# Kernel optimization log

Measured on AMD Instinct MI355X. Metric: run time of the kernel, lower is better.

## Reference

```python
import math
import jax, jax.numpy as jnp
import numpy as np

EMBED_DIM = 512
NUM_HEADS = 8
QHD = 32          # query/key head dim
PHD = 4           # pos head dim (unused: use_pos_scores forced False in source)
IN_PROJ = (QHD + QHD + PHD) * NUM_HEADS  # 544
S = 2048
B = 4
MASK_VAL = -1000.0  # source uses masked_fill(mask, -1000)


def sinusoidal_pe(T, d):
    # PE(pos,2i)=sin(pos/10000^(2i/d)), PE(pos,2i+1)=cos(...)
    pos = jnp.arange(T, dtype=jnp.float32)[:, None]
    div = jnp.exp(jnp.arange(0, d, 2, dtype=jnp.float32) * (-math.log(10000.0) / d))
    pe = jnp.zeros((T, d), jnp.float32)
    pe = pe.at[:, 0::2].set(jnp.sin(pos * div))
    pe = pe.at[:, 1::2].set(jnp.cos(pos * div))
    return pe


def setup_inputs() -> dict:
    key = jax.random.key(0)
    ks = jax.random.split(key, 4)
    scale = QHD ** (-0.25) / math.sqrt(EMBED_DIM)  # ScaledLinear initial_scale folded in
    return {
        "query": jax.random.normal(ks[0], (S, B, EMBED_DIM), jnp.float32),
        "key": jax.random.normal(ks[1], (S, B, EMBED_DIM), jnp.float32),
        "Wq": jax.random.normal(ks[2], (EMBED_DIM, IN_PROJ), jnp.float32) * scale,
        "bq": jnp.zeros((IN_PROJ,), jnp.float32),
        "Wk": jax.random.normal(ks[3], (EMBED_DIM, IN_PROJ), jnp.float32) * scale,
        "bk": jnp.zeros((IN_PROJ,), jnp.float32),
        "key_padding_mask": jnp.zeros((B, S), bool),
        "attn_mask": jnp.zeros((S, S), bool),
    }


def reference(query, key, Wq, bq, Wk, bk, key_padding_mask, attn_mask):
    q_len, batch, _ = query.shape
    k_len = key.shape[0]
    # key_proj over full in_proj_dim (k slice taken below, p slice is dead code)
    k_proj = key @ Wk + bk                       # (K, B, IN_PROJ)
    # decoder_pos: add sinusoidal PE to query (dropout inactive at eval)
    pe = sinusoidal_pe(q_len, EMBED_DIM)
    q_proj = (query + pe[:, None, :]) @ Wq + bq  # (Q, B, IN_PROJ)
    qd = QHD * NUM_HEADS
    q = q_proj[..., :qd].reshape(q_len, batch, NUM_HEADS, QHD)
    k = k_proj[..., qd:2 * qd].reshape(k_len, batch, NUM_HEADS, QHD)
    # attn_scores: (num_heads, batch, q_len, k_len)
    scores = jnp.einsum("qbhd,kbhd->hbqk", q, k)
    scores = jnp.where(attn_mask[None, None, :, :], MASK_VAL, scores)
    scores = jnp.where(key_padding_mask[None, :, None, :], MASK_VAL, scores)
    return jax.nn.softmax(scores, axis=-1)
```

## Files before the change

kernel.cpp:

```cpp
#include <hip/hip_runtime.h>
#include <math.h>

typedef __bf16 bf16_t;
typedef __bf16 bf16x8 __attribute__((ext_vector_type(8)));
typedef __bf16 bf16x4v __attribute__((ext_vector_type(4)));
typedef float f32x4 __attribute__((ext_vector_type(4)));

#define MFMA16x16(a, b, c) __builtin_amdgcn_mfma_f32_16x16x32_bf16((a), (b), (c), 0, 0, 0)

#define MASK_VAL -1000.0f
#define EXP_SHIFT 20.0f


__global__ __launch_bounds__(256) void prep_qpe(const float* __restrict__ query,
                                                bf16_t* __restrict__ qin) {
    int idx = blockIdx.x * 256 + threadIdx.x;
    int s = idx >> 8;
    int i = idx & 255;
    int e = i * 2;
    const float C = 9.210340371976184f / 512.0f;
    float freq = __expf(-(float)e * C);
    float ang = (float)s * freq;
    float sv, cv;
    sincosf(ang, &sv, &cv);
    #pragma unroll
    for (int b = 0; b < 4; b++) {
        int base = ((s * 4 + b) << 9) + e;
        qin[base]     = (bf16_t)(query[base] + sv);
        qin[base + 1] = (bf16_t)(query[base + 1] + cv);
    }
}

__global__ __launch_bounds__(256) void prep_kcast(const float* __restrict__ key,
                                                  bf16_t* __restrict__ kin) {
    int idx = blockIdx.x * 256 + threadIdx.x;
    float4 v = ((const float4*)key)[idx];
    bf16x4v o;
    o.x = (bf16_t)v.x; o.y = (bf16_t)v.y; o.z = (bf16_t)v.z; o.w = (bf16_t)v.w;
    ((bf16x4v*)kin)[idx] = o;
}

__global__ __launch_bounds__(256) void prep_wt(const float* __restrict__ Wq,
                                               const float* __restrict__ Wk,
                                               bf16_t* __restrict__ wqt,
                                               bf16_t* __restrict__ wkt) {
    int idx = blockIdx.x * 256 + threadIdx.x;
    int t = idx & 131071;
    int j = t >> 9, e = t & 511;
    if (idx < 131072) wqt[t] = (bf16_t)Wq[e * 544 + j];
    else              wkt[t] = (bf16_t)Wk[e * 544 + 256 + j];
}

__global__ __launch_bounds__(256) void mask_any(const uint4* __restrict__ am,
                                                const uint4* __restrict__ kpm,
                                                int* __restrict__ flag) {
    int idx = blockIdx.x * 256 + threadIdx.x;
    unsigned int v = 0;
    if (idx < 262144) { uint4 x = am[idx]; v = x.x | x.y | x.z | x.w; }
    else if (idx < 262656) { uint4 x = kpm[idx - 262144]; v = x.x | x.y | x.z | x.w; }
    if (v) atomicOr(flag, 1);
}

__global__ __launch_bounds__(256) void proj_gemm(const bf16_t* __restrict__ A,
                                                 const bf16_t* __restrict__ Bt,
                                                 const float* __restrict__ bias,
                                                 bf16_t* __restrict__ Out) {
    int lane = threadIdx.x & 63;
    int wave = threadIdx.x >> 6;
    int wm = wave & 1, wn = wave >> 1;
    int m0 = blockIdx.x * 64 + wm * 32;
    int n0 = blockIdx.y * 64 + wn * 32;
    int lrow = lane & 15, quad = lane >> 4;
    f32x4 acc00 = {0.f, 0.f, 0.f, 0.f};
    f32x4 acc01 = acc00, acc10 = acc00, acc11 = acc00;
    const bf16_t* Ab = A + (size_t)(m0 + lrow) * 512 + quad * 8;
    const bf16_t* Bb = Bt + (size_t)(n0 + lrow) * 512 + quad * 8;
    #pragma unroll 4
    for (int k0 = 0; k0 < 512; k0 += 32) {
        bf16x8 a0 = *(const bf16x8*)(Ab + k0);
        bf16x8 a1 = *(const bf16x8*)(Ab + 16 * 512 + k0);
        bf16x8 b0 = *(const bf16x8*)(Bb + k0);
        bf16x8 b1 = *(const bf16x8*)(Bb + 16 * 512 + k0);
        acc00 = MFMA16x16(a0, b0, acc00);
        acc01 = MFMA16x16(a0, b1, acc01);
        acc10 = MFMA16x16(a1, b0, acc10);
        acc11 = MFMA16x16(a1, b1, acc11);
    }
    #pragma unroll
    for (int i = 0; i < 2; i++) {
        #pragma unroll
        for (int j = 0; j < 2; j++) {
            f32x4 acc = (i == 0) ? (j == 0 ? acc00 : acc01) : (j == 0 ? acc10 : acc11);
            int col = n0 + j * 16 + lrow;
            float bv = bias[col];
            int h = col >> 5, d = col & 31;
            #pragma unroll
            for (int r = 0; r < 4; r++) {
                int row = m0 + i * 16 + quad * 4 + r;
                int s = row >> 2, bb = row & 3;
                Out[(size_t)((h * 4 + bb) * 2048 + s) * 32 + d] = (bf16_t)(acc[r] + bv);
            }
        }
    }
}

template <bool MASKED>
__device__ __forceinline__ void attn_core(const bf16_t* __restrict__ Qb,
                                          const bf16_t* __restrict__ Kb,
                                          const unsigned char* __restrict__ am,
                                          const unsigned char* __restrict__ kpm,
                                          float* __restrict__ out) {
    int lane = threadIdx.x & 63;
    int wave = threadIdx.x >> 6;
    int hb = blockIdx.y;
    int b = hb & 3;
    int q0 = blockIdx.x * 64 + wave * 16;
    int lrow = lane & 15, quad = lane >> 4;
    bf16x8 afrag = *(const bf16x8*)(Qb + (size_t)(hb * 2048 + q0 + lrow) * 32 + quad * 8);
    const bf16_t* kbase = Kb + (size_t)hb * 2048 * 32;

    float m[4] = {-1e30f, -1e30f, -1e30f, -1e30f};
    float l[4] = {0.f, 0.f, 0.f, 0.f};
    #pragma unroll 2
    for (int t0 = 0; t0 < 2048; t0 += 16) {
        bf16x8 bfrag = *(const bf16x8*)(kbase + (size_t)(t0 + lrow) * 32 + quad * 8);
        f32x4 acc = {0.f, 0.f, 0.f, 0.f};
        acc = MFMA16x16(afrag, bfrag, acc);
        int col = t0 + lrow;
        bool kp = MASKED ? (kpm[b * 2048 + col] != 0) : false;
        #pragma unroll
        for (int r = 0; r < 4; r++) {
            float s = acc[r];
            if (MASKED) {
                int row = q0 + quad * 4 + r;
                if (kp || am[(size_t)row * 2048 + col]) s = MASK_VAL;
            }
            m[r] = fmaxf(m[r], s);
            l[r] += __expf(s - EXP_SHIFT);
        }
    }
    #pragma unroll
    for (int off = 1; off < 16; off <<= 1) {
        #pragma unroll
        for (int r = 0; r < 4; r++) {
            m[r] = fmaxf(m[r], __shfl_xor(m[r], off));
            l[r] += __shfl_xor(l[r], off);
        }
    }
    float M[4], INV[4];
    bool need = false;
    #pragma unroll
    for (int r = 0; r < 4; r++) need = need || (l[r] == 0.0f) || (m[r] > 80.0f);
    if (__any(need)) {
        float l2[4] = {0.f, 0.f, 0.f, 0.f};
        for (int t0 = 0; t0 < 2048; t0 += 16) {
            bf16x8 bfrag = *(const bf16x8*)(kbase + (size_t)(t0 + lrow) * 32 + quad * 8);
            f32x4 acc = {0.f, 0.f, 0.f, 0.f};
            acc = MFMA16x16(afrag, bfrag, acc);
            int col = t0 + lrow;
            bool kp = MASKED ? (kpm[b * 2048 + col] != 0) : false;
            #pragma unroll
            for (int r = 0; r < 4; r++) {
                float s = acc[r];
                if (MASKED) {
                    int row = q0 + quad * 4 + r;
                    if (kp || am[(size_t)row * 2048 + col]) s = MASK_VAL;
                }
                l2[r] += __expf(s - m[r]);
            }
        }
        #pragma unroll
        for (int off = 1; off < 16; off <<= 1) {
            #pragma unroll
            for (int r = 0; r < 4; r++) l2[r] += __shfl_xor(l2[r], off);
        }
        #pragma unroll
        for (int r = 0; r < 4; r++) { M[r] = m[r]; INV[r] = 1.0f / l2[r]; }
    } else {
        #pragma unroll
        for (int r = 0; r < 4; r++) { M[r] = EXP_SHIFT; INV[r] = 1.0f / l[r]; }
    }
    float* obase = out + (size_t)hb * 2048 * 2048;
    #pragma unroll 2
    for (int t0 = 0; t0 < 2048; t0 += 16) {
        bf16x8 bfrag = *(const bf16x8*)(kbase + (size_t)(t0 + lrow) * 32 + quad * 8);
        f32x4 acc = {0.f, 0.f, 0.f, 0.f};
        acc = MFMA16x16(afrag, bfrag, acc);
        int col = t0 + lrow;
        bool kp = MASKED ? (kpm[b * 2048 + col] != 0) : false;
        #pragma unroll
        for (int r = 0; r < 4; r++) {
            float s = acc[r];
            int row = q0 + quad * 4 + r;
            if (MASKED) {
                if (kp || am[(size_t)row * 2048 + col]) s = MASK_VAL;
            }
            float o = __expf(s - M[r]) * INV[r];
            __builtin_nontemporal_store(o, obase + (size_t)row * 2048 + col);
        }
    }
}

__global__ __launch_bounds__(256) void attn_kernel(const bf16_t* __restrict__ Qb,
                                                   const bf16_t* __restrict__ Kb,
                                                   const unsigned char* __restrict__ am,
                                                   const unsigned char* __restrict__ kpm,
                                                   const int* __restrict__ flag,
                                                   float* __restrict__ out) {
    if (*flag) attn_core<true>(Qb, Kb, am, kpm, out);
    else       attn_core<false>(Qb, Kb, am, kpm, out);
}

extern "C" void kernel_launch(void* const* d_in, const int* in_sizes, int n_in,
                              void* d_out, int out_size, void* d_ws, size_t ws_size,
                              hipStream_t stream) {
    const float* query = (const float*)d_in[0];
    const float* key   = (const float*)d_in[1];
    const float* Wq    = (const float*)d_in[2];
    const float* bq    = (const float*)d_in[3];
    const float* Wk    = (const float*)d_in[4];
    const float* bk    = (const float*)d_in[5];
    const unsigned char* kpm = (const unsigned char*)d_in[6];
    const unsigned char* am  = (const unsigned char*)d_in[7];
    float* out = (float*)d_out;

    char* ws = (char*)d_ws;
    bf16_t* qin = (bf16_t*)(ws);
    bf16_t* kin = (bf16_t*)(ws + (8u << 20));
    bf16_t* wqt = (bf16_t*)(ws + (16u << 20));
    bf16_t* wkt = (bf16_t*)(ws + (16u << 20) + (256u << 10));
    bf16_t* Qb  = (bf16_t*)(ws + (17u << 20));
    bf16_t* Kb  = (bf16_t*)(ws + (21u << 20));
    int* flag   = (int*)(ws + (25u << 20));

    hipMemsetAsync(flag, 0, 4, stream);
    prep_qpe<<<2048, 256, 0, stream>>>(query, qin);
    prep_kcast<<<4096, 256, 0, stream>>>(key, kin);
    prep_wt<<<1024, 256, 0, stream>>>(Wq, Wk, wqt, wkt);
    mask_any<<<1026, 256, 0, stream>>>((const uint4*)am, (const uint4*)kpm, flag);
    proj_gemm<<<dim3(128, 4), 256, 0, stream>>>(qin, wqt, bq, Qb);
    proj_gemm<<<dim3(128, 4), 256, 0, stream>>>(kin, wkt, bk + 256, Kb);
    attn_kernel<<<dim3(32, 32), 256, 0, stream>>>(Qb, Kb, am, kpm, flag, out);
}
```

Baseline: 728.9 us.

## Transpose attention MFMA for row-contiguous float4 stores and split masked/unmasked kernels

The score MFMA now uses K as the A operand and Q as B, so each lane owns four consecutive key columns of one query row. Output can then be written as 16-byte nontemporal float4 stores, and mask bytes read as uchar4. Softmax is rewritten with exp2f and a folded log-normalizer, removing the per-element multiply by an inverse. The attention kernel is split into separate no-mask and masked kernels with launch bounds, and prep_qpe is vectorized. The cost is an extra kernel launch whose body exits early.

```diff
diff --git a/kernel.cpp b/kernel.cpp
--- a/kernel.cpp
+++ b/kernel.cpp
@@ -9,26 +9,32 @@
 #define MFMA16x16(a, b, c) __builtin_amdgcn_mfma_f32_16x16x32_bf16((a), (b), (c), 0, 0, 0)
 
 #define MASK_VAL -1000.0f
-#define EXP_SHIFT 20.0f
+#define LOG2E 1.4426950408889634f
+#define SH2 28.853900817779268f
 
 
 __global__ __launch_bounds__(256) void prep_qpe(const float* __restrict__ query,
                                                 bf16_t* __restrict__ qin) {
     int idx = blockIdx.x * 256 + threadIdx.x;
-    int s = idx >> 8;
-    int i = idx & 255;
-    int e = i * 2;
+    int m = idx >> 6;
+    int e0 = (idx & 63) << 3;
+    int s = m >> 2;
     const float C = 9.210340371976184f / 512.0f;
-    float freq = __expf(-(float)e * C);
-    float ang = (float)s * freq;
-    float sv, cv;
-    sincosf(ang, &sv, &cv);
+    const float* qp = query + (size_t)m * 512 + e0;
+    float4 v0 = *(const float4*)qp;
+    float4 v1 = *(const float4*)(qp + 4);
+    float pe[8];
     #pragma unroll
-    for (int b = 0; b < 4; b++) {
-        int base = ((s * 4 + b) << 9) + e;
-        qin[base]     = (bf16_t)(query[base] + sv);
-        qin[base + 1] = (bf16_t)(query[base + 1] + cv);
-    }
+    for (int p = 0; p < 4; p++) {
+        float freq = __expf(-(float)(e0 + 2 * p) * C);
+        sincosf((float)s * freq, &pe[2 * p], &pe[2 * p + 1]);
+    }
+    bf16x8 o;
+    o[0] = (bf16_t)(v0.x + pe[0]); o[1] = (bf16_t)(v0.y + pe[1]);
+    o[2] = (bf16_t)(v0.z + pe[2]); o[3] = (bf16_t)(v0.w + pe[3]);
+    o[4] = (bf16_t)(v1.x + pe[4]); o[5] = (bf16_t)(v1.y + pe[5]);
+    o[6] = (bf16_t)(v1.z + pe[6]); o[7] = (bf16_t)(v1.w + pe[7]);
+    *(bf16x8*)(qin + (size_t)m * 512 + e0) = o;
 }
 
 __global__ __launch_bounds__(256) void prep_kcast(const float* __restrict__ key,
@@ -116,99 +122,99 @@
     int b = hb & 3;
     int q0 = blockIdx.x * 64 + wave * 16;
     int lrow = lane & 15, quad = lane >> 4;
-    bf16x8 afrag = *(const bf16x8*)(Qb + (size_t)(hb * 2048 + q0 + lrow) * 32 + quad * 8);
-    const bf16_t* kbase = Kb + (size_t)hb * 2048 * 32;
-
-    float m[4] = {-1e30f, -1e30f, -1e30f, -1e30f};
-    float l[4] = {0.f, 0.f, 0.f, 0.f};
-    #pragma unroll 2
+    int row = q0 + lrow;
+    bf16x8 qfrag = *(const bf16x8*)(Qb + (size_t)(hb * 2048 + row) * 32 + quad * 8);
+    const bf16_t* kptr = Kb + (size_t)hb * 2048 * 32 + (size_t)lrow * 32 + quad * 8;
+    const unsigned char* amrow = MASKED ? am + (size_t)row * 2048 + quad * 4 : nullptr;
+    const unsigned char* kpmb  = MASKED ? kpm + (size_t)b * 2048 + quad * 4 : nullptr;
+
+    float m = -1e30f, l = 0.f;
+    #pragma unroll 4
     for (int t0 = 0; t0 < 2048; t0 += 16) {
-        bf16x8 bfrag = *(const bf16x8*)(kbase + (size_t)(t0 + lrow) * 32 + quad * 8);
+        bf16x8 kfrag = *(const bf16x8*)(kptr + (size_t)t0 * 32);
         f32x4 acc = {0.f, 0.f, 0.f, 0.f};
-        acc = MFMA16x16(afrag, bfrag, acc);
-        int col = t0 + lrow;
-        bool kp = MASKED ? (kpm[b * 2048 + col] != 0) : false;
-        #pragma unroll
-        for (int r = 0; r < 4; r++) {
-            float s = acc[r];
+        acc = MFMA16x16(kfrag, qfrag, acc);
+        if (MASKED) {
+            uchar4 a4 = *(const uchar4*)(amrow + t0);
+            uchar4 k4 = *(const uchar4*)(kpmb + t0);
+            if (a4.x | k4.x) acc[0] = MASK_VAL;
+            if (a4.y | k4.y) acc[1] = MASK_VAL;
+            if (a4.z | k4.z) acc[2] = MASK_VAL;
+            if (a4.w | k4.w) acc[3] = MASK_VAL;
+        }
+        m = fmaxf(m, fmaxf(fmaxf(acc[0], acc[1]), fmaxf(acc[2], acc[3])));
+        l += exp2f(fmaf(acc[0], LOG2E, -SH2)) + exp2f(fmaf(acc[1], LOG2E, -SH2))
+           + exp2f(fmaf(acc[2], LOG2E, -SH2)) + exp2f(fmaf(acc[3], LOG2E, -SH2));
+    }
+    m = fmaxf(m, __shfl_xor(m, 16)); l += __shfl_xor(l, 16);
+    m = fmaxf(m, __shfl_xor(m, 32)); l += __shfl_xor(l, 32);
+
+    float M2, lf;
+    if (__any((l == 0.0f) || (m > 80.0f))) {
+        float mL = m * LOG2E;
+        float l2 = 0.f;
+        for (int t0 = 0; t0 < 2048; t0 += 16) {
+            bf16x8 kfrag = *(const bf16x8*)(kptr + (size_t)t0 * 32);
+            f32x4 acc = {0.f, 0.f, 0.f, 0.f};
+            acc = MFMA16x16(kfrag, qfrag, acc);
             if (MASKED) {
-                int row = q0 + quad * 4 + r;
-                if (kp || am[(size_t)row * 2048 + col]) s = MASK_VAL;
+                uchar4 a4 = *(const uchar4*)(amrow + t0);
+                uchar4 k4 = *(const uchar4*)(kpmb + t0);
+                if (a4.x | k4.x) acc[0] = MASK_VAL;
+                if (a4.y | k4.y) acc[1] = MASK_VAL;
+                if (a4.z | k4.z) acc[2] = MASK_VAL;
+                if (a4.w | k4.w) acc[3] = MASK_VAL;
             }
-            m[r] = fmaxf(m[r], s);
-            l[r] += __expf(s - EXP_SHIFT);
-        }
-    }
-    #pragma unroll
-    for (int off = 1; off < 16; off <<= 1) {
-        #pragma unroll
-        for (int r = 0; r < 4; r++) {
-            m[r] = fmaxf(m[r], __shfl_xor(m[r], off));
-            l[r] += __shfl_xor(l[r], off);
-        }
-    }
-    float M[4], INV[4];
-    bool need = false;
-    #pragma unroll
-    for (int r = 0; r < 4; r++) need = need || (l[r] == 0.0f) || (m[r] > 80.0f);
-    if (__any(need)) {
-        float l2[4] = {0.f, 0.f, 0.f, 0.f};
-        for (int t0 = 0; t0 < 2048; t0 += 16) {
-            bf16x8 bfrag = *(const bf16x8*)(kbase + (size_t)(t0 + lrow) * 32 + quad * 8);
-            f32x4 acc = {0.f, 0.f, 0.f, 0.f};
-            acc = MFMA16x16(afrag, bfrag, acc);
-            int col = t0 + lrow;
-            bool kp = MASKED ? (kpm[b * 2048 + col] != 0) : false;
-            #pragma unroll
-            for (int r = 0; r < 4; r++) {
-                float s = acc[r];
-                if (MASKED) {
-                    int row = q0 + quad * 4 + r;
-                    if (kp || am[(size_t)row * 2048 + col]) s = MASK_VAL;
-                }
-                l2[r] += __expf(s - m[r]);
-            }
-        }
-        #pragma unroll
-        for (int off = 1; off < 16; off <<= 1) {
-            #pragma unroll
-            for (int r = 0; r < 4; r++) l2[r] += __shfl_xor(l2[r], off);
-        }
-        #pragma unroll
-        for (int r = 0; r < 4; r++) { M[r] = m[r]; INV[r] = 1.0f / l2[r]; }
+            l2 += exp2f(fmaf(acc[0], LOG2E, -mL)) + exp2f(fmaf(acc[1], LOG2E, -mL))
+                + exp2f(fmaf(acc[2], LOG2E, -mL)) + exp2f(fmaf(acc[3], LOG2E, -mL));
+        }
+        l2 += __shfl_xor(l2, 16);
+        l2 += __shfl_xor(l2, 32);
+        M2 = mL; lf = l2;
     } else {
-        #pragma unroll
-        for (int r = 0; r < 4; r++) { M[r] = EXP_SHIFT; INV[r] = 1.0f / l[r]; }
-    }
-    float* obase = out + (size_t)hb * 2048 * 2048;
-    #pragma unroll 2
+        M2 = SH2; lf = l;
+    }
+    float C2 = M2 + log2f(lf);
+
+    float* orow = out + (size_t)hb * 2048 * 2048 + (size_t)row * 2048 + quad * 4;
+    #pragma unroll 4
     for (int t0 = 0; t0 < 2048; t0 += 16) {
-        bf16x8 bfrag = *(const bf16x8*)(kbase + (size_t)(t0 + lrow) * 32 + quad * 8);
+        bf16x8 kfrag = *(const bf16x8*)(kptr + (size_t)t0 * 32);
         f32x4 acc = {0.f, 0.f, 0.f, 0.f};
-        acc = MFMA16x16(afrag, bfrag, acc);
-        int col = t0 + lrow;
-        bool kp = MASKED ? (kpm[b * 2048 + col] != 0) : false;
-        #pragma unroll
-        for (int r = 0; r < 4; r++) {
-            float s = acc[r];
-            int row = q0 + quad * 4 + r;
-            if (MASKED) {
-                if (kp || am[(size_t)row * 2048 + col]) s = MASK_VAL;
-            }
-            float o = __expf(s - M[r]) * INV[r];
-            __builtin_nontemporal_store(o, obase + (size_t)row * 2048 + col);
-        }
-    }
-}
-
-__global__ __launch_bounds__(256) void attn_kernel(const bf16_t* __restrict__ Qb,
+        acc = MFMA16x16(kfrag, qfrag, acc);
+        if (MASKED) {
+            uchar4 a4 = *(const uchar4*)(amrow + t0);
+            uchar4 k4 = *(const uchar4*)(kpmb + t0);
+            if (a4.x | k4.x) acc[0] = MASK_VAL;
+            if (a4.y | k4.y) acc[1] = MASK_VAL;
+            if (a4.z | k4.z) acc[2] = MASK_VAL;
+            if (a4.w | k4.w) acc[3] = MASK_VAL;
+        }
+        f32x4 o;
+        o[0] = exp2f(fmaf(acc[0], LOG2E, -C2));
+        o[1] = exp2f(fmaf(acc[1], LOG2E, -C2));
+        o[2] = exp2f(fmaf(acc[2], LOG2E, -C2));
+        o[3] = exp2f(fmaf(acc[3], LOG2E, -C2));
+        __builtin_nontemporal_store(o, (f32x4*)(orow + t0));
+    }
+}
+
+__global__ __launch_bounds__(256, 4) void attn_nomask(const bf16_t* __restrict__ Qb,
+                                                      const bf16_t* __restrict__ Kb,
+                                                      const int* __restrict__ flag,
+                                                      float* __restrict__ out) {
+    if (*flag) return;
+    attn_core<false>(Qb, Kb, nullptr, nullptr, out);
+}
+
+__global__ __launch_bounds__(256) void attn_masked(const bf16_t* __restrict__ Qb,
                                                    const bf16_t* __restrict__ Kb,
                                                    const unsigned char* __restrict__ am,
                                                    const unsigned char* __restrict__ kpm,
                                                    const int* __restrict__ flag,
                                                    float* __restrict__ out) {
-    if (*flag) attn_core<true>(Qb, Kb, am, kpm, out);
-    else       attn_core<false>(Qb, Kb, am, kpm, out);
+    if (!*flag) return;
+    attn_core<true>(Qb, Kb, am, kpm, out);
 }
 
 extern "C" void kernel_launch(void* const* d_in, const int* in_sizes, int n_in,
@@ -240,5 +246,6 @@
     mask_any<<<1026, 256, 0, stream>>>((const uint4*)am, (const uint4*)kpm, flag);
     proj_gemm<<<dim3(128, 4), 256, 0, stream>>>(qin, wqt, bq, Qb);
     proj_gemm<<<dim3(128, 4), 256, 0, stream>>>(kin, wkt, bk + 256, Kb);
-    attn_kernel<<<dim3(32, 32), 256, 0, stream>>>(Qb, Kb, am, kpm, flag, out);
-}
+    attn_nomask<<<dim3(32, 32), 256, 0, stream>>>(Qb, Kb, flag, out);
+    attn_masked<<<dim3(32, 32), 256, 0, stream>>>(Qb, Kb, am, kpm, flag, out);
+}
```

Result: faster. 709.0 us (-2.7%).
